# Performance work log

Hardware: AMD Instinct MI355X
Metric: run time of the kernel (lower is better)

## Reference

```python
import jax, jax.numpy as jnp
import numpy as np

EMB = 768
HEADS = 12


def setup_inputs() -> dict:
    key = jax.random.key(0)
    ks = jax.random.split(key, 5)
    B, T, C = 4, 2048, EMB
    scale = 0.02
    return {
        "x": jax.random.normal(ks[0], (B, T, C), dtype=jnp.float32),
        "w_qkv": jax.random.normal(ks[1], (C, 3 * C), dtype=jnp.float32) * scale,
        "b_qkv": jnp.zeros((3 * C,), dtype=jnp.float32),
        "w_proj": jax.random.normal(ks[2], (C, C), dtype=jnp.float32) * scale,
        "b_proj": jnp.zeros((C,), dtype=jnp.float32),
    }


def reference(x, w_qkv, b_qkv, w_proj, b_proj):
    B, T, C = x.shape
    H = HEADS
    Dh = C // H
    qkv = x @ w_qkv + b_qkv  # [B,T,3C]
    q, k, v = jnp.split(qkv, 3, axis=-1)
    # [B,H,T,Dh]
    q = q.reshape(B, T, H, Dh).transpose(0, 2, 1, 3)
    k = k.reshape(B, T, H, Dh).transpose(0, 2, 1, 3)
    v = v.reshape(B, T, H, Dh).transpose(0, 2, 1, 3)
    scores = jnp.einsum("bhqd,bhkd->bhqk", q, k) / jnp.sqrt(jnp.float32(Dh))
    causal = jnp.tril(jnp.ones((T, T), dtype=bool))  # [T,T]
    scores = jnp.where(causal, scores, jnp.float32(-jnp.inf))
    attn = jax.nn.softmax(scores, axis=-1)
    y = jnp.einsum("bhqk,bhkd->bhqd", attn, v)  # [B,H,T,Dh]
    y = y.transpose(0, 2, 1, 3).reshape(B, T, C)
    return y @ w_proj + b_proj
```

## Files before the change

### kernel.cpp

```cpp
#include <hip/hip_runtime.h>

typedef __attribute__((ext_vector_type(8))) short short8;
typedef __attribute__((ext_vector_type(4))) float f32x4;
typedef __attribute__((ext_vector_type(4))) unsigned short ushort4v;
typedef unsigned short ushort;

__device__ __forceinline__ ushort f2bf(float f) {
    union { float f; unsigned u; } v; v.f = f;
    unsigned r = v.u + 0x7fff + ((v.u >> 16) & 1);
    return (ushort)(r >> 16);
}

__device__ __forceinline__ short8 bfscale8(short8 v, float s) {
    short8 o;
#pragma unroll
    for (int j = 0; j < 8; j++) {
        union { float f; unsigned u; } t; t.u = ((unsigned)(ushort)v[j]) << 16;
        o[j] = (short)f2bf(t.f * s);
    }
    return o;
}

__device__ __forceinline__ void gload16(const void* g, void* l) {
    __builtin_amdgcn_global_load_lds(
        (const __attribute__((address_space(1))) void*)g,
        (__attribute__((address_space(3))) void*)l, 16, 0, 0);
}

__global__ __launch_bounds__(256) void cvt_kernel(const float* __restrict__ in,
                                                  ushort* __restrict__ out, int n4) {
    int i = blockIdx.x * 256 + threadIdx.x;
    if (i < n4) {
        float4 v = ((const float4*)in)[i];
        ushort4v o;
        o.x = f2bf(v.x); o.y = f2bf(v.y); o.z = f2bf(v.z); o.w = f2bf(v.w);
        ((ushort4v*)out)[i] = o;
    }
}

__global__ __launch_bounds__(256) void tcvt_kernel(const float* __restrict__ in,
                                                   ushort* __restrict__ out, int R, int C0) {
    __shared__ float tile[32][33];
    const int tx = threadIdx.x & 31, ty = threadIdx.x >> 5;
    const int bx = blockIdx.x, by = blockIdx.y;
#pragma unroll
    for (int j = ty; j < 32; j += 8)
        tile[j][tx] = in[(size_t)(by * 32 + j) * C0 + bx * 32 + tx];
    __syncthreads();
#pragma unroll
    for (int j = ty; j < 32; j += 8)
        out[(size_t)(bx * 32 + j) * R + by * 32 + tx] = f2bf(tile[tx][j]);
}

__global__ __launch_bounds__(256) void vtrans_kernel(const ushort* __restrict__ qkv,
                                                     ushort* __restrict__ vt) {
    constexpr int T = 2048, H = 12, CC = 2304;
    const int bh = blockIdx.z;
    const int b = bh / H, h = bh - b * H;
    const int t0 = blockIdx.x * 32, d0 = blockIdx.y * 32;
    __shared__ ushort tile[32][33];
    const int tx = threadIdx.x & 31, ty = threadIdx.x >> 5;
#pragma unroll
    for (int j = ty; j < 32; j += 8)
        tile[j][tx] = qkv[(size_t)(b * T + t0 + j) * CC + 1536 + h * 64 + d0 + tx];
    __syncthreads();
#pragma unroll
    for (int j = ty; j < 32; j += 8)
        vt[((size_t)bh * 64 + d0 + j) * T + t0 + tx] = tile[tx][j];
}

template <bool OUT_F32>
__global__ __launch_bounds__(256)
void gemm128(const ushort* __restrict__ A, const ushort* __restrict__ Bt,
             const float* __restrict__ bias, void* __restrict__ Cout,
             int M, int N, int K) {
    __shared__ __attribute__((aligned(16))) ushort sA[128 * 32];
    __shared__ __attribute__((aligned(16))) ushort sB[128 * 32];
    const int tid = threadIdx.x;
    const int lane = tid & 63, w = tid >> 6;
    const int wm = w >> 1, wn = w & 1;
    const int c = lane & 15, g = lane >> 4;
    const int m0 = blockIdx.x * 128, n0 = blockIdx.y * 128;

    const f32x4 fz = {0.f, 0.f, 0.f, 0.f};
    f32x4 acc[4][4];
#pragma unroll
    for (int i = 0; i < 4; i++)
#pragma unroll
        for (int j = 0; j < 4; j++) acc[i][j] = fz;

    const int e0 = tid * 8, e1 = (256 + tid) * 8;
    const ushort* Ab0 = A + (size_t)(m0 + (e0 >> 5)) * K + (e0 & 31);
    const ushort* Ab1 = A + (size_t)(m0 + (e1 >> 5)) * K + (e1 & 31);
    const ushort* Bb0 = Bt + (size_t)(n0 + (e0 >> 5)) * K + (e0 & 31);
    const ushort* Bb1 = Bt + (size_t)(n0 + (e1 >> 5)) * K + (e1 & 31);

    const int nk = K >> 5;
    for (int kt = 0; kt < nk; ++kt) {
        gload16(Ab0 + kt * 32, &sA[e0]);
        gload16(Ab1 + kt * 32, &sA[e1]);
        gload16(Bb0 + kt * 32, &sB[e0]);
        gload16(Bb1 + kt * 32, &sB[e1]);
        __syncthreads();
        short8 af[4], bfr[4];
#pragma unroll
        for (int mi = 0; mi < 4; mi++)
            af[mi] = *(const short8*)&sA[(wm * 64 + mi * 16 + c) * 32 + g * 8];
#pragma unroll
        for (int ni = 0; ni < 4; ni++)
            bfr[ni] = *(const short8*)&sB[(wn * 64 + ni * 16 + c) * 32 + g * 8];
#pragma unroll
        for (int mi = 0; mi < 4; mi++)
#pragma unroll
            for (int ni = 0; ni < 4; ni++)
                acc[mi][ni] = __builtin_amdgcn_mfma_f32_16x16x32_bf16(
                    af[mi], bfr[ni], acc[mi][ni], 0, 0, 0);
        __syncthreads();
    }

    const int crow = m0 + wm * 64, ccol = n0 + wn * 64;
#pragma unroll
    for (int ni = 0; ni < 4; ni++) {
        const float bv = bias[ccol + ni * 16 + c];
#pragma unroll
        for (int mi = 0; mi < 4; mi++) {
#pragma unroll
            for (int r = 0; r < 4; r++) {
                float v = acc[mi][ni][r] + bv;
                size_t idx = (size_t)(crow + mi * 16 + g * 4 + r) * N + ccol + ni * 16 + c;
                if (OUT_F32) ((float*)Cout)[idx] = v;
                else ((ushort*)Cout)[idx] = f2bf(v);
            }
        }
    }
}

__global__ __launch_bounds__(256)
void attn_fwd(const ushort* __restrict__ qkv, const ushort* __restrict__ vt,
              ushort* __restrict__ outp) {
    constexpr int T = 2048, H = 12, CC = 2304;
    const int bh = blockIdx.y;
    const int b = bh / H, h = bh - b * H;
    const int p = blockIdx.x;
    const int qt_hi = 31 - p, qt_lo = p;
    const int tid = threadIdx.x;
    const int w = tid >> 6, lane = tid & 63;
    const int c = lane & 15, g = lane >> 4;

    __shared__ __attribute__((aligned(16))) ushort sK[2][64 * 64];
    __shared__ __attribute__((aligned(16))) ushort sV[2][64 * 64];
    __shared__ __attribute__((aligned(16))) ushort sP[4][2][16 * 64];

    const int qb[2] = {qt_hi * 64 + w * 16, qt_lo * 64 + w * 16};
    const int qtl[2] = {qt_hi, qt_lo};

    const float SCL = 0.125f * 1.44269504f;
    short8 qf0[2], qf1[2];
#pragma unroll
    for (int ss = 0; ss < 2; ++ss) {
        const ushort* qp = qkv + (size_t)(b * T + qb[ss] + c) * CC + h * 64 + g * 8;
        qf0[ss] = bfscale8(*(const short8*)qp, SCL);
        qf1[ss] = bfscale8(*(const short8*)(qp + 32), SCL);
    }

    const f32x4 fz = {0.f, 0.f, 0.f, 0.f};
    f32x4 accO[2][4];
    f32x4 accL[2];
#pragma unroll
    for (int ss = 0; ss < 2; ++ss) {
        accL[ss] = fz;
#pragma unroll
        for (int ni = 0; ni < 4; ni++) accO[ss][ni] = fz;
    }

    short8 onesf;
    {
        ushort ov = (c == 0) ? (ushort)0x3F80 : (ushort)0;
#pragma unroll
        for (int j = 0; j < 8; j++) onesf[j] = (short)ov;
    }

    const int rowA = w * 8 + (lane >> 3);
    const int rowB = 32 + rowA;
    const int ps0 = lane & 7;
    const ushort* kS0 = qkv + (size_t)(b * T + rowA) * CC + 768 + h * 64 + ((ps0 ^ (rowA & 7)) << 3);
    const ushort* kS1 = qkv + (size_t)(b * T + rowB) * CC + 768 + h * 64 + ((ps0 ^ (rowB & 7)) << 3);
    const ushort* vS0 = vt + ((size_t)bh * 64 + rowA) * T + ((ps0 ^ (rowA & 7)) << 3);
    const ushort* vS1 = vt + ((size_t)bh * 64 + rowB) * T + ((ps0 ^ (rowB & 7)) << 3);
    const int ldK0 = (w * 8) * 64 + lane * 8;
    const int ldK1 = (32 + w * 8) * 64 + lane * 8;

#define STAGE(buf, kv0)                                                          \
    do {                                                                         \
        gload16(kS0 + (size_t)(kv0)*CC, &sK[buf][ldK0]);                         \
        gload16(kS1 + (size_t)(kv0)*CC, &sK[buf][ldK1]);                         \
        gload16(vS0 + (kv0), &sV[buf][ldK0]);                                    \
        gload16(vS1 + (kv0), &sV[buf][ldK1]);                                    \
    } while (0)

    STAGE(0, 0);
    int cur = 0;

    for (int t = 0; t <= qt_hi; ++t) {
        __syncthreads();
        if (t < qt_hi) STAGE(cur ^ 1, (t + 1) * 64);
        const ushort* K_ = &sK[cur][0];
        const ushort* V_ = &sV[cur][0];
        const bool both = (t <= qt_lo);

        f32x4 sc[2][4];
#pragma unroll
        for (int ni = 0; ni < 4; ni++) { sc[0][ni] = fz; sc[1][ni] = fz; }
#pragma unroll
        for (int ni = 0; ni < 4; ni++) {
            const int rw = (ni * 16 + c) * 64;
            short8 kf0 = *(const short8*)&K_[rw + ((g ^ (c & 7)) << 3)];
            short8 kf1 = *(const short8*)&K_[rw + (((4 + g) ^ (c & 7)) << 3)];
            sc[0][ni] = __builtin_amdgcn_mfma_f32_16x16x32_bf16(qf0[0], kf0, sc[0][ni], 0, 0, 0);
            sc[0][ni] = __builtin_amdgcn_mfma_f32_16x16x32_bf16(qf1[0], kf1, sc[0][ni], 0, 0, 0);
            if (both) {
                sc[1][ni] = __builtin_amdgcn_mfma_f32_16x16x32_bf16(qf0[1], kf0, sc[1][ni], 0, 0, 0);
                sc[1][ni] = __builtin_amdgcn_mfma_f32_16x16x32_bf16(qf1[1], kf1, sc[1][ni], 0, 0, 0);
            }
        }

#pragma unroll
        for (int ss = 0; ss < 2; ++ss) {
            if (ss == 1 && !both) continue;
            if (t == qtl[ss]) {
#pragma unroll
                for (int ni = 0; ni < 4; ni++)
#pragma unroll
                    for (int r = 0; r < 4; r++) {
                        const int kvg = t * 64 + ni * 16 + c;
                        const int qg = qb[ss] + g * 4 + r;
                        float sv = (kvg > qg) ? -1e30f : sc[ss][ni][r];
                        float pv = __builtin_amdgcn_exp2f(sv);
                        const int row = g * 4 + r;
                        sP[w][ss][row * 64 + ((((ni << 1) | (c >> 3)) ^ (row & 7)) << 3) + (c & 7)] =
                            f2bf(pv);
                    }
            } else {
#pragma unroll
                for (int ni = 0; ni < 4; ni++)
#pragma unroll
                    for (int r = 0; r < 4; r++) {
                        float pv = __builtin_amdgcn_exp2f(sc[ss][ni][r]);
                        const int row = g * 4 + r;
                        sP[w][ss][row * 64 + ((((ni << 1) | (c >> 3)) ^ (row & 7)) << 3) + (c & 7)] =
                            f2bf(pv);
                    }
            }
        }
        asm volatile("s_waitcnt lgkmcnt(0)" ::: "memory");
        __builtin_amdgcn_sched_barrier(0);

#pragma unroll
        for (int ks = 0; ks < 2; ++ks) {
            short8 pf0 = *(const short8*)&sP[w][0][c * 64 + (((ks * 4 + g) ^ (c & 7)) << 3)];
            short8 pf1;
            if (both) pf1 = *(const short8*)&sP[w][1][c * 64 + (((ks * 4 + g) ^ (c & 7)) << 3)];
#pragma unroll
            for (int ni = 0; ni < 4; ni++) {
                short8 vf = *(const short8*)&V_[(ni * 16 + c) * 64 + (((ks * 4 + g) ^ (c & 7)) << 3)];
                accO[0][ni] = __builtin_amdgcn_mfma_f32_16x16x32_bf16(pf0, vf, accO[0][ni], 0, 0, 0);
                if (both)
                    accO[1][ni] = __builtin_amdgcn_mfma_f32_16x16x32_bf16(pf1, vf, accO[1][ni], 0, 0, 0);
            }
            accL[0] = __builtin_amdgcn_mfma_f32_16x16x32_bf16(pf0, onesf, accL[0], 0, 0, 0);
            if (both)
                accL[1] = __builtin_amdgcn_mfma_f32_16x16x32_bf16(pf1, onesf, accL[1], 0, 0, 0);
        }
        cur ^= 1;
    }
#undef STAGE

#pragma unroll
    for (int ss = 0; ss < 2; ++ss) {
        float linv[4];
#pragma unroll
        for (int r = 0; r < 4; r++) {
            float lv = __shfl(accL[ss][r], lane & 48, 64);
            linv[r] = 1.0f / lv;
        }
#pragma unroll
        for (int ni = 0; ni < 4; ni++)
#pragma unroll
            for (int r = 0; r < 4; r++) {
                float v = accO[ss][ni][r] * linv[r];
                outp[(size_t)(b * T + qb[ss] + g * 4 + r) * 768 + h * 64 + ni * 16 + c] = f2bf(v);
            }
    }
}

extern "C" void kernel_launch(void* const* d_in, const int* in_sizes, int n_in,
                              void* d_out, int out_size, void* d_ws, size_t ws_size,
                              hipStream_t stream) {
    const float* x      = (const float*)d_in[0];
    const float* w_qkv  = (const float*)d_in[1];
    const float* b_qkv  = (const float*)d_in[2];
    const float* w_proj = (const float*)d_in[3];
    const float* b_proj = (const float*)d_in[4];
    float* out = (float*)d_out;

    constexpr int B = 4, T = 2048, C = 768, H = 12;
    constexpr int M = B * T;
    constexpr int N1 = 3 * C;

    char* ws = (char*)d_ws;
    ushort* xb      = (ushort*)(ws);
    ushort* wqkvT   = (ushort*)(ws + 12582912);
    ushort* wprojT  = (ushort*)(ws + 16121856);
    ushort* qkvb    = (ushort*)(ws + 17301504);
    ushort* vtb     = (ushort*)(ws + 55050240);
    ushort* attnout = (ushort*)(ws + 67633152);

    cvt_kernel<<<(M * C / 4 + 255) / 256, 256, 0, stream>>>(x, xb, M * C / 4);
    tcvt_kernel<<<dim3(N1 / 32, C / 32), 256, 0, stream>>>(w_qkv, wqkvT, C, N1);
    tcvt_kernel<<<dim3(C / 32, C / 32), 256, 0, stream>>>(w_proj, wprojT, C, C);
    gemm128<false><<<dim3(M / 128, N1 / 128), 256, 0, stream>>>(xb, wqkvT, b_qkv, qkvb, M, N1, C);
    vtrans_kernel<<<dim3(T / 32, 2, B * H), 256, 0, stream>>>(qkvb, vtb);
    attn_fwd<<<dim3(16, B * H), 256, 0, stream>>>(qkvb, vtb, attnout);
    gemm128<true><<<dim3(M / 128, C / 128), 256, 0, stream>>>(attnout, wprojT, b_proj, out, M, C, C);
}
```

Measured before the change: 230.7 us.

## Keep attention probabilities in registers via transposed QK^T and double-buffer GEMM tiles

In attention, the QK^T MFMA operands are swapped and K rows are permuted so the score accumulator layout already matches the A-operand layout of the PV MFMA. Probabilities are packed to bf16 with v_cvt_pk_bf16_f32 in registers, which removes the shared-memory round trip through sP, its LDS wait, and the scalar conversion. The GEMM gains a second shared-memory buffer so the next K-tile loads while the current one is computed, dropping one barrier per iteration. This costs extra LDS in the GEMM and relies on an intricate lane-to-row mapping that must stay correct.

```diff
diff --git a/kernel.cpp b/kernel.cpp
--- a/kernel.cpp
+++ b/kernel.cpp
@@ -9,6 +9,12 @@
     union { float f; unsigned u; } v; v.f = f;
     unsigned r = v.u + 0x7fff + ((v.u >> 16) & 1);
     return (ushort)(r >> 16);
+}
+
+__device__ __forceinline__ unsigned pkbf(float lo, float hi) {
+    unsigned r;
+    asm("v_cvt_pk_bf16_f32 %0, %1, %2" : "=v"(r) : "v"(lo), "v"(hi));
+    return r;
 }
 
 __device__ __forceinline__ short8 bfscale8(short8 v, float s) {
@@ -74,8 +80,8 @@
 void gemm128(const ushort* __restrict__ A, const ushort* __restrict__ Bt,
              const float* __restrict__ bias, void* __restrict__ Cout,
              int M, int N, int K) {
-    __shared__ __attribute__((aligned(16))) ushort sA[128 * 32];
-    __shared__ __attribute__((aligned(16))) ushort sB[128 * 32];
+    __shared__ __attribute__((aligned(16))) ushort sA[2][128 * 32];
+    __shared__ __attribute__((aligned(16))) ushort sB[2][128 * 32];
     const int tid = threadIdx.x;
     const int lane = tid & 63, w = tid >> 6;
     const int wm = w >> 1, wn = w & 1;
@@ -95,28 +101,35 @@
     const ushort* Bb0 = Bt + (size_t)(n0 + (e0 >> 5)) * K + (e0 & 31);
     const ushort* Bb1 = Bt + (size_t)(n0 + (e1 >> 5)) * K + (e1 & 31);
 
+#define GSTAGE(buf, kt)                                   \
+    do {                                                  \
+        gload16(Ab0 + (kt) * 32, &sA[buf][e0]);           \
+        gload16(Ab1 + (kt) * 32, &sA[buf][e1]);           \
+        gload16(Bb0 + (kt) * 32, &sB[buf][e0]);           \
+        gload16(Bb1 + (kt) * 32, &sB[buf][e1]);           \
+    } while (0)
+
     const int nk = K >> 5;
+    GSTAGE(0, 0);
     for (int kt = 0; kt < nk; ++kt) {
-        gload16(Ab0 + kt * 32, &sA[e0]);
-        gload16(Ab1 + kt * 32, &sA[e1]);
-        gload16(Bb0 + kt * 32, &sB[e0]);
-        gload16(Bb1 + kt * 32, &sB[e1]);
         __syncthreads();
+        if (kt + 1 < nk) GSTAGE((kt + 1) & 1, kt + 1);
+        const int cb = kt & 1;
         short8 af[4], bfr[4];
 #pragma unroll
         for (int mi = 0; mi < 4; mi++)
-            af[mi] = *(const short8*)&sA[(wm * 64 + mi * 16 + c) * 32 + g * 8];
+            af[mi] = *(const short8*)&sA[cb][(wm * 64 + mi * 16 + c) * 32 + g * 8];
 #pragma unroll
         for (int ni = 0; ni < 4; ni++)
-            bfr[ni] = *(const short8*)&sB[(wn * 64 + ni * 16 + c) * 32 + g * 8];
+            bfr[ni] = *(const short8*)&sB[cb][(wn * 64 + ni * 16 + c) * 32 + g * 8];
 #pragma unroll
         for (int mi = 0; mi < 4; mi++)
 #pragma unroll
             for (int ni = 0; ni < 4; ni++)
                 acc[mi][ni] = __builtin_amdgcn_mfma_f32_16x16x32_bf16(
                     af[mi], bfr[ni], acc[mi][ni], 0, 0, 0);
-        __syncthreads();
-    }
+    }
+#undef GSTAGE
 
     const int crow = m0 + wm * 64, ccol = n0 + wn * 64;
 #pragma unroll
@@ -149,7 +162,6 @@
 
     __shared__ __attribute__((aligned(16))) ushort sK[2][64 * 64];
     __shared__ __attribute__((aligned(16))) ushort sV[2][64 * 64];
-    __shared__ __attribute__((aligned(16))) ushort sP[4][2][16 * 64];
 
     const int qb[2] = {qt_hi * 64 + w * 16, qt_lo * 64 + w * 16};
     const int qtl[2] = {qt_hi, qt_lo};
@@ -179,6 +191,14 @@
 #pragma unroll
         for (int j = 0; j < 8; j++) onesf[j] = (short)ov;
     }
+
+    const int a_ = c >> 2, r_ = c & 3;
+    const int rowE = 8 * a_ + r_ + 4 * (a_ & 1);
+    const int rowO = 8 * a_ + r_ + 4 * ((a_ & 1) ^ 1);
+    const int kaE0 = rowE * 64 + ((g ^ (rowE & 7)) << 3);
+    const int kaE1 = rowE * 64 + (((4 + g) ^ (rowE & 7)) << 3);
+    const int kaO0 = rowO * 64 + ((g ^ (rowO & 7)) << 3);
+    const int kaO1 = rowO * 64 + (((4 + g) ^ (rowO & 7)) << 3);
 
     const int rowA = w * 8 + (lane >> 3);
     const int rowB = 32 + rowA;
@@ -190,7 +210,7 @@
     const int ldK0 = (w * 8) * 64 + lane * 8;
     const int ldK1 = (32 + w * 8) * 64 + lane * 8;
 
-#define STAGE(buf, kv0)                                                          \
+#define ASTAGE(buf, kv0)                                                         \
     do {                                                                         \
         gload16(kS0 + (size_t)(kv0)*CC, &sK[buf][ldK0]);                         \
         gload16(kS1 + (size_t)(kv0)*CC, &sK[buf][ldK1]);                         \
@@ -198,12 +218,14 @@
         gload16(vS1 + (kv0), &sV[buf][ldK1]);                                    \
     } while (0)
 
-    STAGE(0, 0);
+    ASTAGE(0, 0);
     int cur = 0;
+
+    union U8 { unsigned u[4]; short8 s; };
 
     for (int t = 0; t <= qt_hi; ++t) {
         __syncthreads();
-        if (t < qt_hi) STAGE(cur ^ 1, (t + 1) * 64);
+        if (t < qt_hi) ASTAGE(cur ^ 1, (t + 1) * 64);
         const ushort* K_ = &sK[cur][0];
         const ushort* V_ = &sV[cur][0];
         const bool both = (t <= qt_lo);
@@ -212,15 +234,17 @@
 #pragma unroll
         for (int ni = 0; ni < 4; ni++) { sc[0][ni] = fz; sc[1][ni] = fz; }
 #pragma unroll
-        for (int ni = 0; ni < 4; ni++) {
-            const int rw = (ni * 16 + c) * 64;
-            short8 kf0 = *(const short8*)&K_[rw + ((g ^ (c & 7)) << 3)];
-            short8 kf1 = *(const short8*)&K_[rw + (((4 + g) ^ (c & 7)) << 3)];
-            sc[0][ni] = __builtin_amdgcn_mfma_f32_16x16x32_bf16(qf0[0], kf0, sc[0][ni], 0, 0, 0);
-            sc[0][ni] = __builtin_amdgcn_mfma_f32_16x16x32_bf16(qf1[0], kf1, sc[0][ni], 0, 0, 0);
+        for (int ni = 0; ni < 4; ++ni) {
+            const int off = (ni >> 1) * 2048;
+            const int a0 = (ni & 1) ? kaO0 : kaE0;
+            const int a1 = (ni & 1) ? kaO1 : kaE1;
+            short8 kf0 = *(const short8*)&K_[off + a0];
+            short8 kf1 = *(const short8*)&K_[off + a1];
+            sc[0][ni] = __builtin_amdgcn_mfma_f32_16x16x32_bf16(kf0, qf0[0], sc[0][ni], 0, 0, 0);
+            sc[0][ni] = __builtin_amdgcn_mfma_f32_16x16x32_bf16(kf1, qf1[0], sc[0][ni], 0, 0, 0);
             if (both) {
-                sc[1][ni] = __builtin_amdgcn_mfma_f32_16x16x32_bf16(qf0[1], kf0, sc[1][ni], 0, 0, 0);
-                sc[1][ni] = __builtin_amdgcn_mfma_f32_16x16x32_bf16(qf1[1], kf1, sc[1][ni], 0, 0, 0);
+                sc[1][ni] = __builtin_amdgcn_mfma_f32_16x16x32_bf16(kf0, qf0[1], sc[1][ni], 0, 0, 0);
+                sc[1][ni] = __builtin_amdgcn_mfma_f32_16x16x32_bf16(kf1, qf1[1], sc[1][ni], 0, 0, 0);
             }
         }
 
@@ -228,40 +252,44 @@
         for (int ss = 0; ss < 2; ++ss) {
             if (ss == 1 && !both) continue;
             if (t == qtl[ss]) {
-#pragma unroll
-                for (int ni = 0; ni < 4; ni++)
-#pragma unroll
-                    for (int r = 0; r < 4; r++) {
-                        const int kvg = t * 64 + ni * 16 + c;
-                        const int qg = qb[ss] + g * 4 + r;
-                        float sv = (kvg > qg) ? -1e30f : sc[ss][ni][r];
-                        float pv = __builtin_amdgcn_exp2f(sv);
-                        const int row = g * 4 + r;
-                        sP[w][ss][row * 64 + ((((ni << 1) | (c >> 3)) ^ (row & 7)) << 3) + (c & 7)] =
-                            f2bf(pv);
-                    }
-            } else {
-#pragma unroll
-                for (int ni = 0; ni < 4; ni++)
-#pragma unroll
-                    for (int r = 0; r < 4; r++) {
-                        float pv = __builtin_amdgcn_exp2f(sc[ss][ni][r]);
-                        const int row = g * 4 + r;
-                        sP[w][ss][row * 64 + ((((ni << 1) | (c >> 3)) ^ (row & 7)) << 3) + (c & 7)] =
-                            f2bf(pv);
-                    }
-            }
-        }
-        asm volatile("s_waitcnt lgkmcnt(0)" ::: "memory");
-        __builtin_amdgcn_sched_barrier(0);
-
+                const int qg = qb[ss] + c;
+#pragma unroll
+                for (int ni = 0; ni < 4; ++ni) {
+                    const int kvb = t * 64 + 8 * g + 4 * ((g & 1) ^ (ni & 1)) + 32 * (ni >> 1);
+#pragma unroll
+                    for (int r = 0; r < 4; ++r)
+                        sc[ss][ni][r] = (kvb + r > qg) ? -1e30f : sc[ss][ni][r];
+                }
+            }
+#pragma unroll
+            for (int ni = 0; ni < 4; ++ni)
+#pragma unroll
+                for (int r = 0; r < 4; ++r)
+                    sc[ss][ni][r] = __builtin_amdgcn_exp2f(sc[ss][ni][r]);
+        }
+
+        const bool godd = (g & 1);
 #pragma unroll
         for (int ks = 0; ks < 2; ++ks) {
-            short8 pf0 = *(const short8*)&sP[w][0][c * 64 + (((ks * 4 + g) ^ (c & 7)) << 3)];
-            short8 pf1;
-            if (both) pf1 = *(const short8*)&sP[w][1][c * 64 + (((ks * 4 + g) ^ (c & 7)) << 3)];
-#pragma unroll
-            for (int ni = 0; ni < 4; ni++) {
+            short8 pf0, pf1;
+            {
+                f32x4 pa = godd ? sc[0][2 * ks + 1] : sc[0][2 * ks];
+                f32x4 pb = godd ? sc[0][2 * ks] : sc[0][2 * ks + 1];
+                U8 u;
+                u.u[0] = pkbf(pa[0], pa[1]); u.u[1] = pkbf(pa[2], pa[3]);
+                u.u[2] = pkbf(pb[0], pb[1]); u.u[3] = pkbf(pb[2], pb[3]);
+                pf0 = u.s;
+            }
+            if (both) {
+                f32x4 pa = godd ? sc[1][2 * ks + 1] : sc[1][2 * ks];
+                f32x4 pb = godd ? sc[1][2 * ks] : sc[1][2 * ks + 1];
+                U8 u;
+                u.u[0] = pkbf(pa[0], pa[1]); u.u[1] = pkbf(pa[2], pa[3]);
+                u.u[2] = pkbf(pb[0], pb[1]); u.u[3] = pkbf(pb[2], pb[3]);
+                pf1 = u.s;
+            }
+#pragma unroll
+            for (int ni = 0; ni < 4; ++ni) {
                 short8 vf = *(const short8*)&V_[(ni * 16 + c) * 64 + (((ks * 4 + g) ^ (c & 7)) << 3)];
                 accO[0][ni] = __builtin_amdgcn_mfma_f32_16x16x32_bf16(pf0, vf, accO[0][ni], 0, 0, 0);
                 if (both)
@@ -273,7 +301,7 @@
         }
         cur ^= 1;
     }
-#undef STAGE
+#undef ASTAGE
 
 #pragma unroll
     for (int ss = 0; ss < 2; ++ss) {
```

After: 219.1 us. 5.0% less time.
